# Optimization experiments

Measured on AMD Instinct MI355X. Metric: run time of the kernel, lower is better.

## Reference

```python
import jax, jax.numpy as jnp
import numpy as np

EPS = 1e-6

def _ln(x):
    # LayerNorm, no affine, eps=1e-6
    mu = jnp.mean(x, axis=-1, keepdims=True)
    var = jnp.mean((x - mu) ** 2, axis=-1, keepdims=True)
    return (x - mu) / jnp.sqrt(var + EPS)

def _attend(q, k, v, mask_add, scale):
    # q,k,v: [B,H,N,D]; mask_add: [B,1,1,N]
    attn = jnp.einsum('bhqd,bhkd->bhqk', q, k) * scale + mask_add
    attn = jax.nn.softmax(attn, axis=-1)
    return jnp.einsum('bhqk,bhkd->bhqd', attn, v)

def setup_inputs() -> dict:
    key = jax.random.key(0)
    ks = jax.random.split(key, 16)
    B, N, C, H = 4, 1024, 1024, 16
    mlp_h = 4 * C
    s = 0.02
    inp = {
        'x': jax.random.normal(ks[0], (B, N, C), jnp.float32),
        'c': jax.random.normal(ks[1], (B, N, C), jnp.float32),
        'mask': jax.random.randint(ks[2], (B, N), 0, 2, jnp.int32),
        # self-attention params
        'sa_qkv_w': jax.random.normal(ks[3], (C, 3 * C), jnp.float32) * s,
        'sa_qkv_b': jnp.zeros((3 * C,), jnp.float32),
        'sa_proj_w': jax.random.normal(ks[4], (C, C), jnp.float32) * s,
        'sa_proj_b': jnp.zeros((C,), jnp.float32),
        # cross-attention params
        'ca_q_w': jax.random.normal(ks[5], (C, C), jnp.float32) * s,
        'ca_q_b': jnp.zeros((C,), jnp.float32),
        'ca_k_w': jax.random.normal(ks[6], (C, C), jnp.float32) * s,
        'ca_k_b': jnp.zeros((C,), jnp.float32),
        'ca_v_w': jax.random.normal(ks[7], (C, C), jnp.float32) * s,
        'ca_v_b': jnp.zeros((C,), jnp.float32),
        'ca_proj_w': jax.random.normal(ks[8], (C, C), jnp.float32) * s,
        'ca_proj_b': jnp.zeros((C,), jnp.float32),
        # MLP params
        'fc1_w': jax.random.normal(ks[9], (C, mlp_h), jnp.float32) * s,
        'fc1_b': jnp.zeros((mlp_h,), jnp.float32),
        'fc2_w': jax.random.normal(ks[10], (mlp_h, C), jnp.float32) * s,
        'fc2_b': jnp.zeros((C,), jnp.float32),
    }
    return inp

def reference(x, c, mask,
              sa_qkv_w, sa_qkv_b, sa_proj_w, sa_proj_b,
              ca_q_w, ca_q_b, ca_k_w, ca_k_b, ca_v_w, ca_v_b, ca_proj_w, ca_proj_b,
              fc1_w, fc1_b, fc2_w, fc2_b):
    B, N, C = x.shape
    H = 16
    D = C // H
    scale = D ** -0.5
    # additive mask: 0 where mask==1, -10000 elsewhere; [B,1,1,N]
    mask_add = jnp.where(mask[:, None, None, :] != 1, -10000.0, 0.0).astype(jnp.float32)

    def split_heads(t):  # [B,N,C] -> [B,H,N,D]
        return t.reshape(B, N, H, D).transpose(0, 2, 1, 3)

    # self-attention
    h = _ln(x)
    qkv = h @ sa_qkv_w + sa_qkv_b  # [B,N,3C]
    q, k, v = (split_heads(t) for t in jnp.split(qkv, 3, axis=-1))
    sa = _attend(q, k, v, mask_add, scale).transpose(0, 2, 1, 3).reshape(B, N, C)
    x = x + sa @ sa_proj_w + sa_proj_b

    # cross-attention
    h = _ln(x)
    q = split_heads(h @ ca_q_w + ca_q_b)
    k = split_heads(c @ ca_k_w + ca_k_b)
    v = split_heads(c @ ca_v_w + ca_v_b)
    ca = _attend(q, k, v, mask_add, scale).transpose(0, 2, 1, 3).reshape(B, N, C)
    x = x + ca @ ca_proj_w + ca_proj_b

    # MLP with exact (erf) GELU, matching nn.GELU() default
    h = _ln(x)
    h = jax.nn.gelu(h @ fc1_w + fc1_b, approximate=False)
    x = x + h @ fc2_w + fc2_b
    return x
```

## Files before the change

kernel.cpp:

```cpp
#include <hip/hip_runtime.h>
#include <hip/hip_bf16.h>
#include <cstdint>

typedef __bf16 bf16;
typedef __bf16 b8v __attribute__((ext_vector_type(8)));
typedef __bf16 b4v __attribute__((ext_vector_type(4)));
typedef float  f32x4 __attribute__((ext_vector_type(4)));

#define MFMA16(a, b, c) __builtin_amdgcn_mfma_f32_16x16x32_bf16((a), (b), (c), 0, 0, 0)

__device__ inline void gload_lds16(const void* g, void* l) {
    __builtin_amdgcn_global_load_lds(
        (const __attribute__((address_space(1))) void*)g,
        (__attribute__((address_space(3))) void*)l, 16, 0, 0);
}

__global__ __launch_bounds__(256) void f32_to_bf16_k(const float* __restrict__ in,
                                                     bf16* __restrict__ out) {
    long i = ((long)blockIdx.x * 256 + threadIdx.x) * 8;
    float4 f0 = *(const float4*)&in[i];
    float4 f1 = *(const float4*)&in[i + 4];
    b8v v;
    v[0] = (bf16)f0.x; v[1] = (bf16)f0.y; v[2] = (bf16)f0.z; v[3] = (bf16)f0.w;
    v[4] = (bf16)f1.x; v[5] = (bf16)f1.y; v[6] = (bf16)f1.z; v[7] = (bf16)f1.w;
    *(b8v*)&out[i] = v;
}

__global__ __launch_bounds__(256) void transpose_w_k(const float* __restrict__ in,
                                                     bf16* __restrict__ out,
                                                     int K, int N) {
    __shared__ bf16 t[64][66];
    const int tn = blockIdx.x * 64, tk = blockIdx.y * 64;
    const int tid = threadIdx.x;
    const int r = tid >> 4, c4 = (tid & 15) * 4;
#pragma unroll
    for (int rr = r; rr < 64; rr += 16) {
        float4 v = *(const float4*)&in[(long)(tk + rr) * N + tn + c4];
        t[rr][c4 + 0] = (bf16)v.x;
        t[rr][c4 + 1] = (bf16)v.y;
        t[rr][c4 + 2] = (bf16)v.z;
        t[rr][c4 + 3] = (bf16)v.w;
    }
    __syncthreads();
    const int n = tid >> 3, k8 = (tid & 7) * 8;
#pragma unroll
    for (int nn = n; nn < 64; nn += 32) {
        b8v v;
#pragma unroll
        for (int j = 0; j < 8; ++j) v[j] = t[k8 + j][nn];
        *(b8v*)&out[(long)(tn + nn) * K + tk + k8] = v;
    }
}

__global__ __launch_bounds__(256) void transpose_v_k(const bf16* __restrict__ vp, int vs,
                                                     bf16* __restrict__ VT) {
    __shared__ bf16 t[64][66];
    const int bh = blockIdx.y;
    const long rowbase = (long)(bh >> 4) * 1024;
    const int hoff = (bh & 15) * 64;
    const int tk = blockIdx.x * 64;
    const int tid = threadIdx.x;
    const int r = tid >> 4, c4 = (tid & 15) * 4;
#pragma unroll
    for (int rr = r; rr < 64; rr += 16) {
        b4v v = *(const b4v*)&vp[(rowbase + tk + rr) * vs + hoff + c4];
        t[rr][c4 + 0] = v[0];
        t[rr][c4 + 1] = v[1];
        t[rr][c4 + 2] = v[2];
        t[rr][c4 + 3] = v[3];
    }
    __syncthreads();
    const int d = tid >> 3, k8 = (tid & 7) * 8;
#pragma unroll
    for (int dd = d; dd < 64; dd += 32) {
        b8v v;
#pragma unroll
        for (int j = 0; j < 8; ++j) v[j] = t[k8 + j][dd];
        *(b8v*)&VT[((long)bh * 64 + dd) * 1024 + tk + k8] = v;
    }
}

__global__ __launch_bounds__(256) void layernorm_k(const float* __restrict__ x,
                                                   bf16* __restrict__ h) {
    int row = blockIdx.x;
    const float* xr = x + (long)row * 1024;
    int tid = threadIdx.x;
    float4 v = ((const float4*)xr)[tid];
    float s = v.x + v.y + v.z + v.w;
    float ss = v.x * v.x + v.y * v.y + v.z * v.z + v.w * v.w;
    for (int m = 1; m < 64; m <<= 1) {
        s += __shfl_xor(s, m);
        ss += __shfl_xor(ss, m);
    }
    __shared__ float sbuf[8];
    int wave = tid >> 6, lane = tid & 63;
    if (lane == 0) { sbuf[wave] = s; sbuf[4 + wave] = ss; }
    __syncthreads();
    s = sbuf[0] + sbuf[1] + sbuf[2] + sbuf[3];
    ss = sbuf[4] + sbuf[5] + sbuf[6] + sbuf[7];
    float mu = s * (1.0f / 1024.0f);
    float var = ss * (1.0f / 1024.0f) - mu * mu;
    float rstd = rsqrtf(var + 1e-6f);
    b4v o;
    o[0] = (bf16)((v.x - mu) * rstd);
    o[1] = (bf16)((v.y - mu) * rstd);
    o[2] = (bf16)((v.z - mu) * rstd);
    o[3] = (bf16)((v.w - mu) * rstd);
    *(b4v*)&h[(long)row * 1024 + tid * 4] = o;
}

template <int EPI, int WM>
__global__ __launch_bounds__(256, 2) void gemm_bt(const bf16* __restrict__ A,
                                                  const bf16* __restrict__ Bt,
                                                  const float* __restrict__ bias,
                                                  const float* __restrict__ bias2,
                                                  int nsplit,
                                                  bf16* __restrict__ outb,
                                                  float* __restrict__ res,
                                                  int M, int N, int K) {
    constexpr int BM = WM * 32;
    __shared__ __align__(16) bf16 As[BM * 32];
    __shared__ __align__(16) bf16 Bs[128 * 32];
    const int tid = threadIdx.x;
    const int wave = tid >> 6, lane = tid & 63;
    const int quad = lane >> 4, l16 = lane & 15;
    const int bm = blockIdx.y, bn = blockIdx.x;
    const int wm = wave >> 1, wn = wave & 1;

    f32x4 acc[WM][4] = {};
    const long Abase = (long)bm * BM * K;
    const long Bbase = (long)bn * 128 * K;

    for (int k0 = 0; k0 < K; k0 += 32) {
        __syncthreads();
#pragma unroll
        for (int it = 0; it < BM / 64; ++it) {
            int chunk = it * 256 + tid;
            int row = chunk >> 2, col = (chunk & 3) << 3;
            gload_lds16(A + Abase + (long)row * K + k0 + col,
                        (char*)As + it * 4096 + wave * 1024);
        }
#pragma unroll
        for (int it = 0; it < 2; ++it) {
            int chunk = it * 256 + tid;
            int row = chunk >> 2, col = (chunk & 3) << 3;
            gload_lds16(Bt + Bbase + (long)row * K + k0 + col,
                        (char*)Bs + it * 4096 + wave * 1024);
        }
        __syncthreads();
        b8v a[WM], b[4];
#pragma unroll
        for (int i = 0; i < WM; ++i)
            a[i] = *(const b8v*)&As[(wm * WM * 16 + i * 16 + l16) * 32 + quad * 8];
#pragma unroll
        for (int i = 0; i < 4; ++i)
            b[i] = *(const b8v*)&Bs[(wn * 64 + i * 16 + l16) * 32 + quad * 8];
#pragma unroll
        for (int im = 0; im < WM; ++im)
#pragma unroll
            for (int in = 0; in < 4; ++in)
                acc[im][in] = MFMA16(a[im], b[in], acc[im][in]);
    }

    const int rbase = bm * BM + wm * WM * 16;
    const int cbase = bn * 128 + wn * 64;
#pragma unroll
    for (int in = 0; in < 4; ++in) {
        int col = cbase + in * 16 + l16;
        float bv = (col < nsplit) ? bias[col] : bias2[col - nsplit];
#pragma unroll
        for (int im = 0; im < WM; ++im) {
            int row0 = rbase + im * 16 + quad * 4;
#pragma unroll
            for (int r = 0; r < 4; ++r) {
                long off = (long)(row0 + r) * N + col;
                float v = acc[im][in][r] + bv;
                if (EPI == 0) {
                    outb[off] = (bf16)v;
                } else if (EPI == 1) {
                    res[off] += v;
                } else {
                    v = 0.5f * v * (1.0f + erff(v * 0.70710678118654752f));
                    outb[off] = (bf16)v;
                }
            }
        }
    }
}

__global__ __launch_bounds__(256) void attn_k(const bf16* __restrict__ qp, int qs,
                                              const bf16* __restrict__ kp, int ks,
                                              const bf16* __restrict__ VT,
                                              const int* __restrict__ mask,
                                              bf16* __restrict__ outp) {
    const int bh = blockIdx.y;
    const int b = bh >> 4, hidx = bh & 15;
    const int qt = blockIdx.x;
    const int tid = threadIdx.x;
    const int wave = tid >> 6, lane = tid & 63;
    const int quad = lane >> 4, l16 = lane & 15;

    __shared__ __align__(16) bf16 Qs[64 * 64];
    __shared__ __align__(16) bf16 Ks[64 * 64];
    __shared__ __align__(16) bf16 Vs[64 * 72];
    __shared__ __align__(16) bf16 Ps[4][16 * 72];
    __shared__ float madd_s[1024];

    const int hoff = hidx * 64;
    const long rowbase = (long)b * 1024;

    {
        int4 mv = *(const int4*)&mask[b * 1024 + tid * 4];
        float4 mf;
        mf.x = (mv.x != 1) ? -10000.0f : 0.0f;
        mf.y = (mv.y != 1) ? -10000.0f : 0.0f;
        mf.z = (mv.z != 1) ? -10000.0f : 0.0f;
        mf.w = (mv.w != 1) ? -10000.0f : 0.0f;
        *(float4*)&madd_s[tid * 4] = mf;
    }
    for (int i = tid; i < 512; i += 256) {
        int rr = i >> 3, cc = (i & 7) << 3;
        *(b8v*)&Qs[rr * 64 + cc] = *(const b8v*)&qp[(rowbase + qt * 64 + rr) * qs + hoff + cc];
    }
    __syncthreads();
    b8v qf[2];
    qf[0] = *(const b8v*)&Qs[(wave * 16 + l16) * 64 + quad * 8];
    qf[1] = *(const b8v*)&Qs[(wave * 16 + l16) * 64 + 32 + quad * 8];

    float l_acc[4] = {};
    f32x4 o[4] = {};
    const float scale = 0.125f;

    for (int kt = 0; kt < 16; ++kt) {
        __syncthreads();
        for (int i = tid; i < 512; i += 256) {
            int rr = i >> 3, cc = (i & 7) << 3;
            *(b8v*)&Ks[rr * 64 + cc] = *(const b8v*)&kp[(rowbase + kt * 64 + rr) * ks + hoff + cc];
            *(b8v*)&Vs[rr * 72 + cc] = *(const b8v*)&VT[((long)bh * 64 + rr) * 1024 + kt * 64 + cc];
        }
        __syncthreads();

#pragma unroll
        for (int f = 0; f < 4; ++f) {
            f32x4 acc = {};
            b8v kf0 = *(const b8v*)&Ks[(f * 16 + l16) * 64 + quad * 8];
            b8v kf1 = *(const b8v*)&Ks[(f * 16 + l16) * 64 + 32 + quad * 8];
            acc = MFMA16(qf[0], kf0, acc);
            acc = MFMA16(qf[1], kf1, acc);
            float madd = madd_s[kt * 64 + f * 16 + l16];
#pragma unroll
            for (int r = 0; r < 4; ++r) {
                float p = __expf(acc[r] * scale + madd);
                l_acc[r] += p;
                Ps[wave][(quad * 4 + r) * 72 + f * 16 + l16] = (bf16)p;
            }
        }
        b8v pf0 = *(const b8v*)&Ps[wave][l16 * 72 + quad * 8];
        b8v pf1 = *(const b8v*)&Ps[wave][l16 * 72 + 32 + quad * 8];

#pragma unroll
        for (int f = 0; f < 4; ++f) {
            f32x4 t = o[f];
            b8v vf0 = *(const b8v*)&Vs[(f * 16 + l16) * 72 + quad * 8];
            b8v vf1 = *(const b8v*)&Vs[(f * 16 + l16) * 72 + 32 + quad * 8];
            t = MFMA16(pf0, vf0, t);
            t = MFMA16(pf1, vf1, t);
            o[f] = t;
        }
    }

#pragma unroll
    for (int m = 1; m < 16; m <<= 1)
#pragma unroll
        for (int r = 0; r < 4; ++r) l_acc[r] += __shfl_xor(l_acc[r], m);
    float rinv[4];
#pragma unroll
    for (int r = 0; r < 4; ++r) rinv[r] = 1.0f / l_acc[r];

#pragma unroll
    for (int f = 0; f < 4; ++f)
#pragma unroll
        for (int r = 0; r < 4; ++r) {
            int row = qt * 64 + wave * 16 + quad * 4 + r;
            int col = hoff + f * 16 + l16;
            outp[(rowbase + row) * 1024 + col] = (bf16)(o[f][r] * rinv[r]);
        }
}

extern "C" void kernel_launch(void* const* d_in, const int* in_sizes, int n_in,
                              void* d_out, int out_size, void* d_ws, size_t ws_size,
                              hipStream_t stream) {
    const float* x = (const float*)d_in[0];
    const float* c = (const float*)d_in[1];
    const int* mask = (const int*)d_in[2];
    const float* qkv_w = (const float*)d_in[3];
    const float* qkv_b = (const float*)d_in[4];
    const float* sap_w = (const float*)d_in[5];
    const float* sap_b = (const float*)d_in[6];
    const float* caq_w = (const float*)d_in[7], *caq_b = (const float*)d_in[8];
    const float* cak_w = (const float*)d_in[9], *cak_b = (const float*)d_in[10];
    const float* cav_w = (const float*)d_in[11], *cav_b = (const float*)d_in[12];
    const float* cap_w = (const float*)d_in[13], *cap_b = (const float*)d_in[14];
    const float* fc1_w = (const float*)d_in[15], *fc1_b = (const float*)d_in[16];
    const float* fc2_w = (const float*)d_in[17], *fc2_b = (const float*)d_in[18];

    float* xf = (float*)d_out;

    char* ws = (char*)d_ws;
    bf16* wT = (bf16*)ws;
    bf16* qkvT = wT;
    bf16* sapT = wT + 3145728;
    bf16* caqT = wT + 4194304;
    bf16* cakvT = wT + 5242880;
    bf16* capT = wT + 7340032;
    bf16* fc1T = wT + 8388608;
    bf16* fc2T = wT + 12582912;
    bf16* h    = (bf16*)(ws + (32L << 20));
    bf16* VT   = h;
    bf16* att  = (bf16*)(ws + (40L << 20));
    bf16* qkv  = (bf16*)(ws + (48L << 20));
    bf16* q2   = (bf16*)(ws + (48L << 20));
    bf16* k2v2 = (bf16*)(ws + (56L << 20));
    bf16* gel  = (bf16*)(ws + (48L << 20));
    bf16* cbf  = (bf16*)(ws + (72L << 20));

    transpose_w_k<<<dim3(48, 16), 256, 0, stream>>>(qkv_w, qkvT, 1024, 3072);
    transpose_w_k<<<dim3(16, 16), 256, 0, stream>>>(sap_w, sapT, 1024, 1024);
    transpose_w_k<<<dim3(16, 16), 256, 0, stream>>>(caq_w, caqT, 1024, 1024);
    transpose_w_k<<<dim3(16, 16), 256, 0, stream>>>(cak_w, cakvT, 1024, 1024);
    transpose_w_k<<<dim3(16, 16), 256, 0, stream>>>(cav_w, cakvT + 1048576, 1024, 1024);
    transpose_w_k<<<dim3(16, 16), 256, 0, stream>>>(cap_w, capT, 1024, 1024);
    transpose_w_k<<<dim3(64, 16), 256, 0, stream>>>(fc1_w, fc1T, 1024, 4096);
    transpose_w_k<<<dim3(16, 64), 256, 0, stream>>>(fc2_w, fc2T, 4096, 1024);

    f32_to_bf16_k<<<2048, 256, 0, stream>>>(c, cbf);
    hipMemcpyAsync(xf, x, 4096L * 1024 * 4, hipMemcpyDeviceToDevice, stream);

    layernorm_k<<<4096, 256, 0, stream>>>(xf, h);
    gemm_bt<0, 4><<<dim3(24, 32), 256, 0, stream>>>(h, qkvT, qkv_b, qkv_b, 3072, qkv, nullptr, 4096, 3072, 1024);
    transpose_v_k<<<dim3(16, 64), 256, 0, stream>>>(qkv + 2048, 3072, VT);
    attn_k<<<dim3(16, 64), 256, 0, stream>>>(qkv, 3072, qkv + 1024, 3072, VT, mask, att);
    gemm_bt<1, 2><<<dim3(8, 64), 256, 0, stream>>>(att, sapT, sap_b, sap_b, 1024, nullptr, xf, 4096, 1024, 1024);

    layernorm_k<<<4096, 256, 0, stream>>>(xf, h);
    gemm_bt<0, 2><<<dim3(8, 64), 256, 0, stream>>>(h, caqT, caq_b, caq_b, 1024, q2, nullptr, 4096, 1024, 1024);
    gemm_bt<0, 4><<<dim3(16, 32), 256, 0, stream>>>(cbf, cakvT, cak_b, cav_b, 1024, k2v2, nullptr, 4096, 2048, 1024);
    transpose_v_k<<<dim3(16, 64), 256, 0, stream>>>(k2v2 + 1024, 2048, VT);
    attn_k<<<dim3(16, 64), 256, 0, stream>>>(q2, 1024, k2v2, 2048, VT, mask, att);
    gemm_bt<1, 2><<<dim3(8, 64), 256, 0, stream>>>(att, capT, cap_b, cap_b, 1024, nullptr, xf, 4096, 1024, 1024);

    layernorm_k<<<4096, 256, 0, stream>>>(xf, h);
    gemm_bt<2, 4><<<dim3(32, 32), 256, 0, stream>>>(h, fc1T, fc1_b, fc1_b, 4096, gel, nullptr, 4096, 4096, 1024);
    gemm_bt<1, 2><<<dim3(8, 64), 256, 0, stream>>>(gel, fc2T, fc2_b, fc2_b, 1024, nullptr, xf, 4096, 1024, 4096);
}
```

Measured before the change: 562.8 us.

## Remap GEMM and attention blocks per XCD and load Q/K via direct-to-LDS

Replaces the 2D grids of the GEMM and attention kernels with a 1D grid and remaps block indices so that round-robin XCD dispatch places blocks sharing the same A row-stripe, or the same batch-head, on the same XCD. This aims to improve L2 reuse of shared operand tiles across the MI355X's separate per-XCD caches. The attention kernel also loads its Q and K tiles with global_load_lds, which skips the register round trip. The remapping assumes the M-tile count and batch-head count divide evenly by 8.

```diff
diff --git a/kernel.cpp b/kernel.cpp
--- a/kernel.cpp
+++ b/kernel.cpp
@@ -124,7 +124,15 @@
     const int tid = threadIdx.x;
     const int wave = tid >> 6, lane = tid & 63;
     const int quad = lane >> 4, l16 = lane & 15;
-    const int bm = blockIdx.y, bn = blockIdx.x;
+
+    const int nbm = M / BM;
+    const int stripe = nbm >> 3;
+    const int l = blockIdx.x;
+    const int xcd = l & 7;
+    const int j = l >> 3;
+    const int bm = xcd * stripe + (j % stripe);
+    const int bn = j / stripe;
+
     const int wm = wave >> 1, wn = wave & 1;
 
     f32x4 acc[WM][4] = {};
@@ -193,9 +201,12 @@
                                               const bf16* __restrict__ VT,
                                               const int* __restrict__ mask,
                                               bf16* __restrict__ outp) {
-    const int bh = blockIdx.y;
+    const int l = blockIdx.x;
+    const int xcd = l & 7;
+    const int j = l >> 3;
+    const int bh = xcd * 8 + (j & 7);
+    const int qt = j >> 3;
     const int b = bh >> 4, hidx = bh & 15;
-    const int qt = blockIdx.x;
     const int tid = threadIdx.x;
     const int wave = tid >> 6, lane = tid & 63;
     const int quad = lane >> 4, l16 = lane & 15;
@@ -218,9 +229,12 @@
         mf.w = (mv.w != 1) ? -10000.0f : 0.0f;
         *(float4*)&madd_s[tid * 4] = mf;
     }
-    for (int i = tid; i < 512; i += 256) {
-        int rr = i >> 3, cc = (i & 7) << 3;
-        *(b8v*)&Qs[rr * 64 + cc] = *(const b8v*)&qp[(rowbase + qt * 64 + rr) * qs + hoff + cc];
+#pragma unroll
+    for (int it = 0; it < 2; ++it) {
+        int chunk = it * 256 + tid;
+        int rr = chunk >> 3, cc = (chunk & 7) << 3;
+        gload_lds16(&qp[(rowbase + qt * 64 + rr) * qs + hoff + cc],
+                    (char*)Qs + it * 4096 + wave * 1024);
     }
     __syncthreads();
     b8v qf[2];
@@ -233,9 +247,12 @@
 
     for (int kt = 0; kt < 16; ++kt) {
         __syncthreads();
-        for (int i = tid; i < 512; i += 256) {
-            int rr = i >> 3, cc = (i & 7) << 3;
-            *(b8v*)&Ks[rr * 64 + cc] = *(const b8v*)&kp[(rowbase + kt * 64 + rr) * ks + hoff + cc];
+#pragma unroll
+        for (int it = 0; it < 2; ++it) {
+            int chunk = it * 256 + tid;
+            int rr = chunk >> 3, cc = (chunk & 7) << 3;
+            gload_lds16(&kp[(rowbase + kt * 64 + rr) * ks + hoff + cc],
+                        (char*)Ks + it * 4096 + wave * 1024);
             *(b8v*)&Vs[rr * 72 + cc] = *(const b8v*)&VT[((long)bh * 64 + rr) * 1024 + kt * 64 + cc];
         }
         __syncthreads();
@@ -337,19 +354,19 @@
     hipMemcpyAsync(xf, x, 4096L * 1024 * 4, hipMemcpyDeviceToDevice, stream);
 
     layernorm_k<<<4096, 256, 0, stream>>>(xf, h);
-    gemm_bt<0, 4><<<dim3(24, 32), 256, 0, stream>>>(h, qkvT, qkv_b, qkv_b, 3072, qkv, nullptr, 4096, 3072, 1024);
+    gemm_bt<0, 4><<<24 * 32, 256, 0, stream>>>(h, qkvT, qkv_b, qkv_b, 3072, qkv, nullptr, 4096, 3072, 1024);
     transpose_v_k<<<dim3(16, 64), 256, 0, stream>>>(qkv + 2048, 3072, VT);
-    attn_k<<<dim3(16, 64), 256, 0, stream>>>(qkv, 3072, qkv + 1024, 3072, VT, mask, att);
-    gemm_bt<1, 2><<<dim3(8, 64), 256, 0, stream>>>(att, sapT, sap_b, sap_b, 1024, nullptr, xf, 4096, 1024, 1024);
+    attn_k<<<1024, 256, 0, stream>>>(qkv, 3072, qkv + 1024, 3072, VT, mask, att);
+    gemm_bt<1, 2><<<8 * 64, 256, 0, stream>>>(att, sapT, sap_b, sap_b, 1024, nullptr, xf, 4096, 1024, 1024);
 
     layernorm_k<<<4096, 256, 0, stream>>>(xf, h);
-    gemm_bt<0, 2><<<dim3(8, 64), 256, 0, stream>>>(h, caqT, caq_b, caq_b, 1024, q2, nullptr, 4096, 1024, 1024);
-    gemm_bt<0, 4><<<dim3(16, 32), 256, 0, stream>>>(cbf, cakvT, cak_b, cav_b, 1024, k2v2, nullptr, 4096, 2048, 1024);
+    gemm_bt<0, 2><<<8 * 64, 256, 0, stream>>>(h, caqT, caq_b, caq_b, 1024, q2, nullptr, 4096, 1024, 1024);
+    gemm_bt<0, 4><<<16 * 32, 256, 0, stream>>>(cbf, cakvT, cak_b, cav_b, 1024, k2v2, nullptr, 4096, 2048, 1024);
     transpose_v_k<<<dim3(16, 64), 256, 0, stream>>>(k2v2 + 1024, 2048, VT);
-    attn_k<<<dim3(16, 64), 256, 0, stream>>>(q2, 1024, k2v2, 2048, VT, mask, att);
-    gemm_bt<1, 2><<<dim3(8, 64), 256, 0, stream>>>(att, capT, cap_b, cap_b, 1024, nullptr, xf, 4096, 1024, 1024);
+    attn_k<<<1024, 256, 0, stream>>>(q2, 1024, k2v2, 2048, VT, mask, att);
+    gemm_bt<1, 2><<<8 * 64, 256, 0, stream>>>(att, capT, cap_b, cap_b, 1024, nullptr, xf, 4096, 1024, 1024);
 
     layernorm_k<<<4096, 256, 0, stream>>>(xf, h);
-    gemm_bt<2, 4><<<dim3(32, 32), 256, 0, stream>>>(h, fc1T, fc1_b, fc1_b, 4096, gel, nullptr, 4096, 4096, 1024);
-    gemm_bt<1, 2><<<dim3(8, 64), 256, 0, stream>>>(gel, fc2T, fc2_b, fc2_b, 1024, nullptr, xf, 4096, 1024, 4096);
-}
+    gemm_bt<2, 4><<<32 * 32, 256, 0, stream>>>(h, fc1T, fc1_b, fc1_b, 4096, gel, nullptr, 4096, 4096, 1024);
+    gemm_bt<1, 2><<<8 * 64, 256, 0, stream>>>(gel, fc2T, fc2_b, fc2_b, 1024, nullptr, xf, 4096, 1024, 4096);
+}
```

New measurement: 555.3 us. No clear change (-1.3%).
